# Kernel optimization log

Measured on AMD Instinct MI355X. Metric: run time of the kernel, lower is better.

## Reference

```python
import jax, jax.numpy as jnp
import numpy as np

B, C, HID, H, W = 4, 64, 64, 64, 64


def setup_inputs() -> dict:
    key = jax.random.key(0)
    ks = jax.random.split(key, 9)
    s_in = 1.0 / np.sqrt(C)
    return {
        "x": jax.random.normal(ks[0], (B, C, H, W), dtype=jnp.float32),
        "Wq": jax.random.normal(ks[1], (HID, C), dtype=jnp.float32) * s_in,
        "bq": jnp.zeros((HID,), dtype=jnp.float32),
        "Wk": jax.random.normal(ks[2], (HID, C), dtype=jnp.float32) * s_in,
        "bk": jnp.zeros((HID,), dtype=jnp.float32),
        "Wv": jax.random.normal(ks[3], (C, C), dtype=jnp.float32) * s_in,
        "bv": jnp.zeros((C,), dtype=jnp.float32),
        "Wo": jax.random.normal(ks[4], (1, C), dtype=jnp.float32) * s_in,
        "bo": jnp.zeros((1,), dtype=jnp.float32),
    }


def reference(x, Wq, bq, Wk, bk, Wv, bv, Wo, bo):
    b, c, h, w = x.shape
    n = h * w
    xf = x.reshape(b, c, n)                                   # [B,C,N]
    q = jnp.einsum('dc,bcn->bnd', Wq, xf) + bq                # [B,N,HID]
    k = jnp.einsum('dc,bcn->bdn', Wk, xf) + bk[None, :, None]  # [B,HID,N]
    v = jnp.einsum('ec,bcn->bne', Wv, xf) + bv                # [B,N,C]
    scale = 1.0 / jnp.sqrt(jnp.asarray(k.shape[1], x.dtype))
    attn = jax.nn.softmax(jnp.einsum('bnd,bdm->bnm', q, k) * scale, axis=-1)
    out = jnp.einsum('bnm,bme->bne', attn, v)                 # [B,N,C]
    out = out.transpose(0, 2, 1).reshape(b, c, h, w)
    y = jnp.einsum('oc,bchw->bohw', Wo, out) + bo[None, :, None, None]
    return jax.nn.sigmoid(y)
```

## Files before the change

kernel.cpp:

```cpp
#include <hip/hip_runtime.h>
#include <math.h>

#define NB 4
#define NN 4096
#define QSCALE 0.1803368801f

#define KS 8
#define KPB 512
#define KPW 128
#define NTILES 8
#define NG 4

typedef __bf16 bf16x8 __attribute__((ext_vector_type(8)));
typedef float f32x4 __attribute__((ext_vector_type(4)));

union BF8 { unsigned short u[8]; bf16x8 v; uint4 q; };

static __device__ inline unsigned short f2bf(float f) {
    union { float f; unsigned u; } v; v.f = f;
    unsigned r = v.u + 0x7fffu + ((v.u >> 16) & 1u);
    return (unsigned short)(r >> 16);
}

__global__ __launch_bounds__(256) void prep_mfma(
    const float* __restrict__ x,
    const float* __restrict__ Wq, const float* __restrict__ bq,
    const float* __restrict__ Wk, const float* __restrict__ bk,
    const float* __restrict__ Wv, const float* __restrict__ bv,
    const float* __restrict__ Wo,
    unsigned short* __restrict__ Qb, unsigned short* __restrict__ Kb,
    float* __restrict__ VW)
{
    __shared__ float xt[64 * 33];
    __shared__ float wve_s[64];
    __shared__ unsigned short rows[4 * 16 * 72];

    const int blk = blockIdx.x;
    const int b = blk >> 7;
    const int n0 = (blk & 127) << 5;
    const int tid = threadIdx.x;
    const int wid = tid >> 6, lane = tid & 63;
    const int lg = lane >> 4, ll = lane & 15;

    const float* xb = x + (size_t)b * 64 * NN;
    #pragma unroll
    for (int it = 0; it < 8; ++it) {
        int idx = it * 256 + tid;
        int c = idx >> 5, n = idx & 31;
        xt[c * 33 + n] = xb[(size_t)c * NN + n0 + n];
    }
    {
        int c = tid >> 2, part = tid & 3;
        float a = 0.f;
        #pragma unroll
        for (int j = 0; j < 16; ++j) {
            int e = part * 16 + j;
            a = fmaf(Wo[e], Wv[e * 64 + c], a);
        }
        a += __shfl_xor(a, 1);
        a += __shfl_xor(a, 2);
        if (part == 0) wve_s[c] = a;
    }
    float cv;
    {
        float p = Wo[lane] * bv[lane];
        #pragma unroll
        for (int off = 1; off < 64; off <<= 1) p += __shfl_xor(p, off);
        cv = p;
    }
    __syncthreads();

    {
        int nrel = tid >> 3, part = tid & 7;
        float a = 0.f;
        #pragma unroll
        for (int j = 0; j < 8; ++j) {
            int c = part * 8 + j;
            a = fmaf(wve_s[c], xt[c * 33 + nrel], a);
        }
        a += __shfl_xor(a, 1);
        a += __shfl_xor(a, 2);
        a += __shfl_xor(a, 4);
        if (part == 0) VW[(size_t)b * NN + n0 + nrel] = a + cv;
    }

    const int nr = (wid & 1) * 16 + ll;
    BF8 a0, a1;
    #pragma unroll
    for (int j = 0; j < 8; ++j) {
        a0.v[j] = (__bf16)xt[(lg * 8 + j) * 33 + nr];
        a1.v[j] = (__bf16)xt[(32 + lg * 8 + j) * 33 + nr];
    }

    const float* W  = (wid < 2) ? Wq : Wk;
    const float* bs = (wid < 2) ? bq : bk;
    unsigned short* Out = (wid < 2) ? Qb : Kb;
    const float scale = (wid < 2) ? QSCALE : 1.f;
    unsigned short* myrows = rows + wid * (16 * 72);

    #pragma unroll
    for (int ct = 0; ct < 4; ++ct) {
        const float* wr = W + (ct * 16 + ll) * 64;
        float4 f0 = *(const float4*)(wr + lg * 8);
        float4 f1 = *(const float4*)(wr + lg * 8 + 4);
        float4 f2 = *(const float4*)(wr + 32 + lg * 8);
        float4 f3 = *(const float4*)(wr + 32 + lg * 8 + 4);
        BF8 w0, w1;
        w0.v[0] = (__bf16)f0.x; w0.v[1] = (__bf16)f0.y; w0.v[2] = (__bf16)f0.z; w0.v[3] = (__bf16)f0.w;
        w0.v[4] = (__bf16)f1.x; w0.v[5] = (__bf16)f1.y; w0.v[6] = (__bf16)f1.z; w0.v[7] = (__bf16)f1.w;
        w1.v[0] = (__bf16)f2.x; w1.v[1] = (__bf16)f2.y; w1.v[2] = (__bf16)f2.z; w1.v[3] = (__bf16)f2.w;
        w1.v[4] = (__bf16)f3.x; w1.v[5] = (__bf16)f3.y; w1.v[6] = (__bf16)f3.z; w1.v[7] = (__bf16)f3.w;
        f32x4 acc = {0.f, 0.f, 0.f, 0.f};
        acc = __builtin_amdgcn_mfma_f32_16x16x32_bf16(a0.v, w0.v, acc, 0, 0, 0);
        acc = __builtin_amdgcn_mfma_f32_16x16x32_bf16(a1.v, w1.v, acc, 0, 0, 0);
        float bias = bs[ct * 16 + ll];
        #pragma unroll
        for (int r = 0; r < 4; ++r)
            myrows[(lg * 4 + r) * 72 + ct * 16 + ll] = f2bf((acc[r] + bias) * scale);
    }
    {
        int n = lane >> 2, c16 = lane & 3;
        const uint4* sp = (const uint4*)&myrows[n * 72 + c16 * 16];
        uint4 v0 = sp[0], v1 = sp[1];
        uint4* dst = (uint4*)(Out + ((size_t)b * NN + n0 + (wid & 1) * 16 + n) * 64 + c16 * 16);
        dst[0] = v0; dst[1] = v1;
    }
}

__global__ __launch_bounds__(256) void attn_mfma(
    const unsigned short* __restrict__ Qb, const unsigned short* __restrict__ Kb,
    const float* __restrict__ VW, float2* __restrict__ P2)
{
    __shared__ unsigned short qlds[64 * 72];
    __shared__ float vws[KPB];
    const int blk = blockIdx.x;
    const int ks = blk & (KS - 1);
    const int t = blk >> 3;
    const int b = t >> 6;
    const int q0 = (t & 63) << 6;
    const int tid = threadIdx.x;
    const int wid = tid >> 6, lane = tid & 63;
    const int lg = lane >> 4, ll = lane & 15;

    {
        const uint4* src = (const uint4*)(Qb + ((size_t)b * NN + q0) * 64);
        #pragma unroll
        for (int k = 0; k < 2; ++k) {
            int idx = tid + k * 256;
            int row = idx >> 3, c8 = idx & 7;
            uint4 v = src[idx];
            *(uint4*)&qlds[row * 72 + c8 * 8] = v;
        }
    }
    for (int i = tid; i < KPB; i += 256)
        vws[i] = VW[(size_t)b * NN + ks * KPB + i];
    __syncthreads();

    const unsigned short* kp =
        Kb + ((size_t)b * NN + ks * KPB + wid * KPW + ll) * 64 + lg * 8;

    float Zg[NG], Ag[NG];
    #pragma unroll
    for (int g = 0; g < NG; ++g) { Zg[g] = 0.f; Ag[g] = 0.f; }

    #pragma unroll
    for (int kt = 0; kt < NTILES; ++kt) {
        const bf16x8 ka0 = *(const bf16x8*)(kp + kt * (16 * 64));
        const bf16x8 ka1 = *(const bf16x8*)(kp + kt * (16 * 64) + 32);
        const float4 vv = *(const float4*)&vws[wid * KPW + kt * 16 + lg * 4];
        #pragma unroll
        for (int g = 0; g < NG; ++g) {
            const bf16x8 qa = *(const bf16x8*)&qlds[(g * 16 + ll) * 72 + lg * 8];
            const bf16x8 qc = *(const bf16x8*)&qlds[(g * 16 + ll) * 72 + 32 + lg * 8];
            f32x4 acc = {0.f, 0.f, 0.f, 0.f};
            acc = __builtin_amdgcn_mfma_f32_16x16x32_bf16(ka0, qa, acc, 0, 0, 0);
            acc = __builtin_amdgcn_mfma_f32_16x16x32_bf16(ka1, qc, acc, 0, 0, 0);
            float e0 = __builtin_amdgcn_exp2f(acc[0]);
            float e1 = __builtin_amdgcn_exp2f(acc[1]);
            float e2 = __builtin_amdgcn_exp2f(acc[2]);
            float e3 = __builtin_amdgcn_exp2f(acc[3]);
            Zg[g] += (e0 + e1) + (e2 + e3);
            Ag[g] += fmaf(e0, vv.x, fmaf(e1, vv.y, fmaf(e2, vv.z, e3 * vv.w)));
        }
    }

    #pragma unroll
    for (int g = 0; g < NG; ++g) {
        Zg[g] += __shfl_xor(Zg[g], 16);
        Zg[g] += __shfl_xor(Zg[g], 32);
        Ag[g] += __shfl_xor(Ag[g], 16);
        Ag[g] += __shfl_xor(Ag[g], 32);
    }
    const int r = ks * 4 + wid;
    float Zo = (lg == 0) ? Zg[0] : (lg == 1) ? Zg[1] : (lg == 2) ? Zg[2] : Zg[3];
    float Ao = (lg == 0) ? Ag[0] : (lg == 1) ? Ag[1] : (lg == 2) ? Ag[2] : Ag[3];
    P2[((size_t)r << 14) + ((size_t)b << 12) + q0 + lane] = make_float2(Zo, Ao);
}

__global__ __launch_bounds__(64) void combine_kernel(
    const float2* __restrict__ P2, const float* __restrict__ bo,
    float* __restrict__ out)
{
    int i = blockIdx.x * 64 + threadIdx.x;
    float Z = 0.f, A = 0.f;
    #pragma unroll
    for (int r = 0; r < 32; ++r) {
        float2 p = P2[((size_t)r << 14) + i];
        Z += p.x; A += p.y;
    }
    float y = A / Z + bo[0];
    out[i] = 1.f / (1.f + __expf(-y));
}

extern "C" void kernel_launch(void* const* d_in, const int* in_sizes, int n_in,
                              void* d_out, int out_size, void* d_ws, size_t ws_size,
                              hipStream_t stream)
{
    const float* x  = (const float*)d_in[0];
    const float* Wq = (const float*)d_in[1];
    const float* bq = (const float*)d_in[2];
    const float* Wk = (const float*)d_in[3];
    const float* bk = (const float*)d_in[4];
    const float* Wv = (const float*)d_in[5];
    const float* bv = (const float*)d_in[6];
    const float* Wo = (const float*)d_in[7];
    const float* bo = (const float*)d_in[8];
    float* out = (float*)d_out;

    unsigned short* Qb = (unsigned short*)d_ws;
    unsigned short* Kb = Qb + (size_t)NB * NN * 64;
    float* VW = (float*)(Kb + (size_t)NB * NN * 64);
    float2* P2 = (float2*)(VW + (size_t)NB * NN);

    prep_mfma<<<NB * 128, 256, 0, stream>>>(x, Wq, bq, Wk, bk, Wv, bv, Wo, Qb, Kb, VW);
    attn_mfma<<<NB * 64 * KS, 256, 0, stream>>>(Qb, Kb, VW, P2);
    combine_kernel<<<(NB * NN) / 64, 64, 0, stream>>>(P2, bo, out);
}
```

Before: 37.89 us.

## Keep Q fragments in registers, use packed FMA accumulation, raise occupancy

The attention kernel no longer stages the Q tile in LDS. Each wave loads its Q fragments straight from global memory into registers, which drops the LDS copy and the per-iteration LDS reads. The Z and A accumulations are merged into packed two-wide FMAs (weights {1, v}) so the backend can emit packed-math instructions. The launch bounds now request six blocks per SM and the k-loop unrolls by 2 instead of fully, trading some register pressure and load-latency hiding for occupancy.

```diff
diff --git a/kernel.cpp b/kernel.cpp
--- a/kernel.cpp
+++ b/kernel.cpp
@@ -8,11 +8,12 @@
 #define KS 8
 #define KPB 512
 #define KPW 128
-#define NTILES 8
+#define NTW 8
 #define NG 4
 
 typedef __bf16 bf16x8 __attribute__((ext_vector_type(8)));
 typedef float f32x4 __attribute__((ext_vector_type(4)));
+typedef float f32x2 __attribute__((ext_vector_type(2)));
 
 union BF8 { unsigned short u[8]; bf16x8 v; uint4 q; };
 
@@ -127,11 +128,10 @@
     }
 }
 
-__global__ __launch_bounds__(256) void attn_mfma(
+__global__ __launch_bounds__(256, 6) void attn_mfma(
     const unsigned short* __restrict__ Qb, const unsigned short* __restrict__ Kb,
     const float* __restrict__ VW, float2* __restrict__ P2)
 {
-    __shared__ unsigned short qlds[64 * 72];
     __shared__ float vws[KPB];
     const int blk = blockIdx.x;
     const int ks = blk & (KS - 1);
@@ -142,54 +142,54 @@
     const int wid = tid >> 6, lane = tid & 63;
     const int lg = lane >> 4, ll = lane & 15;
 
-    {
-        const uint4* src = (const uint4*)(Qb + ((size_t)b * NN + q0) * 64);
-        #pragma unroll
-        for (int k = 0; k < 2; ++k) {
-            int idx = tid + k * 256;
-            int row = idx >> 3, c8 = idx & 7;
-            uint4 v = src[idx];
-            *(uint4*)&qlds[row * 72 + c8 * 8] = v;
-        }
-    }
     for (int i = tid; i < KPB; i += 256)
         vws[i] = VW[(size_t)b * NN + ks * KPB + i];
     __syncthreads();
 
+    bf16x8 qfa[NG], qfb[NG];
+    #pragma unroll
+    for (int g = 0; g < NG; ++g) {
+        const unsigned short* qp = Qb + ((size_t)b * NN + q0 + g * 16 + ll) * 64 + lg * 8;
+        qfa[g] = *(const bf16x8*)qp;
+        qfb[g] = *(const bf16x8*)(qp + 32);
+    }
     const unsigned short* kp =
         Kb + ((size_t)b * NN + ks * KPB + wid * KPW + ll) * 64 + lg * 8;
 
-    float Zg[NG], Ag[NG];
-    #pragma unroll
-    for (int g = 0; g < NG; ++g) { Zg[g] = 0.f; Ag[g] = 0.f; }
-
-    #pragma unroll
-    for (int kt = 0; kt < NTILES; ++kt) {
-        const bf16x8 ka0 = *(const bf16x8*)(kp + kt * (16 * 64));
-        const bf16x8 ka1 = *(const bf16x8*)(kp + kt * (16 * 64) + 32);
+    f32x2 ZA[NG];
+    #pragma unroll
+    for (int g = 0; g < NG; ++g) ZA[g] = (f32x2){0.f, 0.f};
+
+    #pragma unroll 2
+    for (int kt = 0; kt < NTW; ++kt) {
+        const bf16x8 ka0 = *(const bf16x8*)(kp + (size_t)kt * (16 * 64));
+        const bf16x8 ka1 = *(const bf16x8*)(kp + (size_t)kt * (16 * 64) + 32);
         const float4 vv = *(const float4*)&vws[wid * KPW + kt * 16 + lg * 4];
+        const f32x2 w0 = {1.f, vv.x}, w1 = {1.f, vv.y};
+        const f32x2 w2 = {1.f, vv.z}, w3 = {1.f, vv.w};
         #pragma unroll
         for (int g = 0; g < NG; ++g) {
-            const bf16x8 qa = *(const bf16x8*)&qlds[(g * 16 + ll) * 72 + lg * 8];
-            const bf16x8 qc = *(const bf16x8*)&qlds[(g * 16 + ll) * 72 + 32 + lg * 8];
             f32x4 acc = {0.f, 0.f, 0.f, 0.f};
-            acc = __builtin_amdgcn_mfma_f32_16x16x32_bf16(ka0, qa, acc, 0, 0, 0);
-            acc = __builtin_amdgcn_mfma_f32_16x16x32_bf16(ka1, qc, acc, 0, 0, 0);
+            acc = __builtin_amdgcn_mfma_f32_16x16x32_bf16(ka0, qfa[g], acc, 0, 0, 0);
+            acc = __builtin_amdgcn_mfma_f32_16x16x32_bf16(ka1, qfb[g], acc, 0, 0, 0);
             float e0 = __builtin_amdgcn_exp2f(acc[0]);
             float e1 = __builtin_amdgcn_exp2f(acc[1]);
             float e2 = __builtin_amdgcn_exp2f(acc[2]);
             float e3 = __builtin_amdgcn_exp2f(acc[3]);
-            Zg[g] += (e0 + e1) + (e2 + e3);
-            Ag[g] += fmaf(e0, vv.x, fmaf(e1, vv.y, fmaf(e2, vv.z, e3 * vv.w)));
+            ZA[g] = __builtin_elementwise_fma((f32x2){e0, e0}, w0, ZA[g]);
+            ZA[g] = __builtin_elementwise_fma((f32x2){e1, e1}, w1, ZA[g]);
+            ZA[g] = __builtin_elementwise_fma((f32x2){e2, e2}, w2, ZA[g]);
+            ZA[g] = __builtin_elementwise_fma((f32x2){e3, e3}, w3, ZA[g]);
         }
     }
 
+    float Zg[NG], Ag[NG];
     #pragma unroll
     for (int g = 0; g < NG; ++g) {
-        Zg[g] += __shfl_xor(Zg[g], 16);
-        Zg[g] += __shfl_xor(Zg[g], 32);
-        Ag[g] += __shfl_xor(Ag[g], 16);
-        Ag[g] += __shfl_xor(Ag[g], 32);
+        float Z = ZA[g].x, A = ZA[g].y;
+        Z += __shfl_xor(Z, 16); Z += __shfl_xor(Z, 32);
+        A += __shfl_xor(A, 16); A += __shfl_xor(A, 32);
+        Zg[g] = Z; Ag[g] = A;
     }
     const int r = ks * 4 + wid;
     float Zo = (lg == 0) ? Zg[0] : (lg == 1) ? Zg[1] : (lg == 2) ? Zg[2] : Zg[3];
```

Result: slower. 44.54 us (+17.5%).
